# Kernel optimization log

Hardware: AMD Instinct MI355X
Metric: run time of the kernel (lower is better)

## Reference

```python
import jax, jax.numpy as jnp
import numpy as np

S = 4096      # seq_len
D = 1024      # d_model
H = 16        # n_heads
E = 64        # head dim (D // H)
SCALE0 = 1.0 / np.sqrt(E)  # sh_scale_factor


def setup_inputs() -> dict:
    key = jax.random.key(0)
    ks = jax.random.split(key, 10)
    std = 1.0 / np.sqrt(D)
    inputs = jax.random.normal(ks[0], (S, D), dtype=jnp.float32)
    # per-head projection weights stacked over heads: [H, D, E]
    Wq = jax.random.normal(ks[1], (H, D, E), dtype=jnp.float32) * std
    bq = jnp.zeros((H, E), dtype=jnp.float32)
    Wk = jax.random.normal(ks[2], (H, D, E), dtype=jnp.float32) * std
    bk = jnp.zeros((H, E), dtype=jnp.float32)
    Wv = jax.random.normal(ks[3], (H, D, E), dtype=jnp.float32) * std
    bv = jnp.zeros((H, E), dtype=jnp.float32)
    # learned per-head scalar scale, initialized to 1/sqrt(E)
    scale = jnp.full((H,), SCALE0, dtype=jnp.float32)
    # output projection (stored as [D_in, D_out])
    Wo = jax.random.normal(ks[4], (H * E, D), dtype=jnp.float32) * std
    bo = jnp.zeros((D,), dtype=jnp.float32)
    return {"inputs": inputs, "Wq": Wq, "bq": bq, "Wk": Wk, "bk": bk,
            "Wv": Wv, "bv": bv, "scale": scale, "Wo": Wo, "bo": bo}


def reference(inputs, Wq, bq, Wk, bk, Wv, bv, scale, Wo, bo):
    # per-head QKV projections, batched over heads: [H, S, E]
    q = jnp.einsum('sd,hde->hse', inputs, Wq) + bq[:, None, :]
    k = jnp.einsum('sd,hde->hse', inputs, Wk) + bk[:, None, :]
    v = jnp.einsum('sd,hde->hse', inputs, Wv) + bv[:, None, :]
    # scores [H, S, S], learned scalar scale per head, softmax over keys
    scores = jnp.einsum('hqe,hke->hqk', q, k) * scale[:, None, None]
    attn = jax.nn.softmax(scores, axis=-1)
    o = jnp.einsum('hqk,hke->hqe', attn, v)           # [H, S, E]
    o = jnp.transpose(o, (1, 0, 2)).reshape(S, H * E)  # concat heads on dim 1
    return o @ Wo + bo                                 # [S, D]
```

## Files before the change

kernel.cpp:

```cpp
#include <hip/hip_runtime.h>
#include <stdint.h>

#define S_LEN 4096
#define D_MOD 1024
#define NH    16
#define EH    64

typedef short bf16x8 __attribute__((ext_vector_type(8)));
typedef float f32x4  __attribute__((ext_vector_type(4)));
typedef float f32x16 __attribute__((ext_vector_type(16)));

__device__ __forceinline__ unsigned short f2b(float x){
    uint32_t u = __float_as_uint(x);
    u = (u + 0x7fffu + ((u >> 16) & 1u)) >> 16;
    return (unsigned short)u;
}

__device__ __forceinline__ uint32_t cvtpk_bf16(float lo, float hi){
    uint32_t r;
    asm volatile("v_cvt_pk_bf16_f32 %0, %1, %2" : "=v"(r) : "v"(lo), "v"(hi));
    return r;
}

__device__ __forceinline__ void gld_lds16(const void* g, void* l){
    __builtin_amdgcn_global_load_lds((const __attribute__((address_space(1))) void*)g,
                                     (__attribute__((address_space(3))) void*)l, 16, 0, 0);
}

#define PSWAP_U(a, b) asm volatile("v_permlane32_swap_b32 %0, %1" : "+v"(a), "+v"(b))

__device__ __forceinline__ float vcopy(float x){
    float y;
    asm volatile("v_mov_b32 %0, %1" : "=v"(y) : "v"(x));
    return y;
}
__device__ __forceinline__ float pswap_add(float x){
    uint32_t a = __float_as_uint(x), b = __float_as_uint(vcopy(x));
    PSWAP_U(a, b);
    return __uint_as_float(a) + __uint_as_float(b);
}

#define WAITV4() asm volatile("s_waitcnt vmcnt(4)" ::: "memory")
#define WAITV0() asm volatile("s_waitcnt vmcnt(0)" ::: "memory")
#define CFENCE() asm volatile("" ::: "memory")


__global__ void k_conv_all(const float* __restrict__ x, unsigned short* __restrict__ xb,
                           const float* __restrict__ Wq, const float* __restrict__ Wk,
                           const float* __restrict__ Wv, unsigned short* __restrict__ wt,
                           const float* __restrict__ Wo, unsigned short* __restrict__ wot){
    __shared__ float lt[64][65];
    const int tid = threadIdx.x;
    int b = blockIdx.x;
    if (b < 4096){
        int i = (b * 256 + tid) * 4;
        float4 v = *(const float4*)(x + i);
        ushort4 o;
        o.x = f2b(v.x); o.y = f2b(v.y); o.z = f2b(v.z); o.w = f2b(v.w);
        *(ushort4*)(xb + i) = o;
        return;
    }
    b -= 4096;
    if (b < 768){
        const int d0 = (b & 15) * 64;
        const int th = b >> 4;
        const int t = th >> 4, h = th & 15;
        const float* W = (t == 0) ? Wq : ((t == 1) ? Wk : Wv);
        #pragma unroll
        for (int i = 0; i < 16; i++){
            int idx = tid + 256 * i;
            int dl = idx >> 6, e = idx & 63;
            lt[dl][e] = W[((size_t)((h << 10) + d0 + dl) << 6) + e];
        }
        __syncthreads();
        #pragma unroll
        for (int i = 0; i < 16; i++){
            int idx = tid + 256 * i;
            int eo = idx >> 6, dlo = idx & 63;
            wt[((size_t)((t << 10) + (h << 6) + eo) << 10) + d0 + dlo] = f2b(lt[dlo][eo]);
        }
    } else {
        b -= 768;
        const int he0 = (b & 15) * 64, d0 = (b >> 4) * 64;
        #pragma unroll
        for (int i = 0; i < 16; i++){
            int idx = tid + 256 * i;
            int r = idx >> 6, c = idx & 63;
            lt[r][c] = Wo[((size_t)(he0 + r) << 10) + d0 + c];
        }
        __syncthreads();
        #pragma unroll
        for (int i = 0; i < 16; i++){
            int idx = tid + 256 * i;
            int rr = idx >> 6, cc = idx & 63;
            wot[((size_t)(d0 + rr) << 10) + he0 + cc] = f2b(lt[cc][rr]);
        }
    }
}

__global__ void k_tv(const unsigned short* __restrict__ vr, unsigned short* __restrict__ vt){
    __shared__ unsigned short lt[64][66];
    const int tid = threadIdx.x;
    const int s0 = blockIdx.x * 64, h = blockIdx.y;
    #pragma unroll
    for (int i = 0; i < 4; i++){
        int idx = tid + 256 * i;
        int r = idx >> 4, c4 = idx & 15;
        ushort4 v = *(const ushort4*)(vr + (((size_t)(h << 12) + s0 + r) << 6) + c4 * 4);
        lt[r][c4 * 4 + 0] = v.x; lt[r][c4 * 4 + 1] = v.y;
        lt[r][c4 * 4 + 2] = v.z; lt[r][c4 * 4 + 3] = v.w;
    }
    __syncthreads();
    #pragma unroll
    for (int i = 0; i < 4; i++){
        int idx = tid + 256 * i;
        int e = idx >> 4, j4 = idx & 15;
        ushort4 o;
        o.x = lt[j4 * 4 + 0][e]; o.y = lt[j4 * 4 + 1][e];
        o.z = lt[j4 * 4 + 2][e]; o.w = lt[j4 * 4 + 3][e];
        *(ushort4*)(vt + (size_t)((h << 6) + e) * 4096 + s0 + j4 * 4) = o;
    }
}


template<int MODE, int NI>
__global__ __launch_bounds__(256, 4)
void k_gemm(const unsigned short* __restrict__ A, const unsigned short* __restrict__ B, int K,
            unsigned short* __restrict__ qb, unsigned short* __restrict__ kb,
            unsigned short* __restrict__ vr,
            const float* __restrict__ b0, const float* __restrict__ b1, const float* __restrict__ b2,
            const float* __restrict__ scl,
            float* __restrict__ outp, const float* __restrict__ bo){
    __shared__ uint4 lsA4[1024];
    __shared__ uint4 lsB4[NI * 256];
    char* lsA = (char*)lsA4;
    char* lsB = (char*)lsB4;
    const int tid = threadIdx.x;
    const int lane = tid & 63, w = tid >> 6;
    const int lr = lane & 15, lg = lane >> 4;
    const int wm = w >> 1, wn = w & 1;

    const int nwg = gridDim.x * gridDim.y;
    int wgid = blockIdx.y * gridDim.x + blockIdx.x;
    wgid = (wgid & 7) * (nwg >> 3) + (wgid >> 3);
    const int bx = wgid % gridDim.x, by = wgid / gridDim.x;

    const int m0 = by * 128, n0 = bx * (32 * NI);
    const int wbase = tid & ~63;

    f32x4 acc[4][NI] = {};

    for (int k0 = 0; k0 < K; k0 += 64){
        __syncthreads();
        #pragma unroll
        for (int i = 0; i < 4; i++){
            int s = tid + 256 * i;
            int row = s >> 3, c = s & 7;
            int cs = c ^ (row & 7);
            gld_lds16(A + (size_t)(m0 + row) * K + k0 + cs * 8, lsA + (wbase + 256 * i) * 16);
        }
        #pragma unroll
        for (int i = 0; i < NI; i++){
            int s = tid + 256 * i;
            int row = s >> 3, c = s & 7;
            int cs = c ^ (row & 7);
            gld_lds16(B + (size_t)(n0 + row) * K + k0 + cs * 8, lsB + (wbase + 256 * i) * 16);
        }
        __syncthreads();
        #pragma unroll
        for (int kc = 0; kc < 2; kc++){
            bf16x8 af[4], bf[NI];
            #pragma unroll
            for (int mi = 0; mi < 4; mi++){
                int row = wm * 64 + mi * 16 + lr;
                int j = kc * 4 + lg;
                af[mi] = *(const bf16x8*)(lsA + row * 128 + (j ^ (row & 7)) * 16);
            }
            #pragma unroll
            for (int ni = 0; ni < NI; ni++){
                int row = wn * (NI * 16) + ni * 16 + lr;
                int j = kc * 4 + lg;
                bf[ni] = *(const bf16x8*)(lsB + row * 128 + (j ^ (row & 7)) * 16);
            }
            #pragma unroll
            for (int mi = 0; mi < 4; mi++)
                #pragma unroll
                for (int ni = 0; ni < NI; ni++)
                    acc[mi][ni] = __builtin_amdgcn_mfma_f32_16x16x32_bf16(af[mi], bf[ni], acc[mi][ni], 0, 0, 0);
        }
    }

    #pragma unroll
    for (int mi = 0; mi < 4; mi++){
        #pragma unroll
        for (int ni = 0; ni < NI; ni++){
            int gnb = n0 + wn * (NI * 16) + ni * 16;
            if (MODE == 0){
                int t = gnb >> 10, h = (gnb >> 6) & 15;
                int e = (gnb & 63) + lr;
                const float* bp = (t == 0) ? b0 : ((t == 1) ? b1 : b2);
                float badd = bp[(h << 6) + e];
                float qs = (t == 0) ? scl[h] * 1.4426950408889634f : 1.0f;
                unsigned short* tgt = (t == 0) ? qb : ((t == 1) ? kb : vr);
                #pragma unroll
                for (int r = 0; r < 4; r++){
                    int gm = m0 + wm * 64 + mi * 16 + lg * 4 + r;
                    tgt[((size_t)((h << 12) + gm) << 6) + e] = f2b((acc[mi][ni][r] + badd) * qs);
                }
            } else {
                int gn = gnb + lr;
                float badd = bo[gn];
                #pragma unroll
                for (int r = 0; r < 4; r++){
                    int gm = m0 + wm * 64 + mi * 16 + lg * 4 + r;
                    outp[(size_t)gm * 1024 + gn] = acc[mi][ni][r] + badd;
                }
            }
        }
    }
}


__global__ __launch_bounds__(256, 2)
void k_attn(const unsigned short* __restrict__ qb, const unsigned short* __restrict__ kb,
            const unsigned short* __restrict__ vt,
            unsigned short* __restrict__ po0, unsigned short* __restrict__ po1,
            float* __restrict__ pl){
    __shared__ uint4 ldsb[2048];
    char* ldsc = (char*)ldsb;

    const int tid = threadIdx.x;
    const int lane = tid & 63, w = tid >> 6;
    const int ql = lane & 31, hi = lane >> 5;

    int wg = blockIdx.y * 32 + blockIdx.x;
    wg = (wg & 7) * 64 + (wg >> 3);
    const int h = wg >> 5;
    const int rem = wg & 31;
    const int qblk = rem >> 1, sk = rem & 1;
    const int q0 = qblk * 256 + w * 64;
    const int kbase = sk * 2048;

    bf16x8 qf0[4], qf1[4];
    #pragma unroll
    for (int kc = 0; kc < 4; kc++){
        qf0[kc] = *(const bf16x8*)(qb + (size_t)((h << 12) + q0 + ql) * 64 + kc * 16 + hi * 8);
        qf1[kc] = *(const bf16x8*)(qb + (size_t)((h << 12) + q0 + 32 + ql) * 64 + kc * 16 + hi * 8);
    }

    f32x16 o00 = {}, o01 = {}, o10 = {}, o11 = {};
    float ps0 = 0.f, ps1 = 0.f;

    auto stage = [&](int buf, int kt){
        char* Kd = ldsc + buf * 16384;
        char* Vd = Kd + 8192;
        #pragma unroll
        for (int c = 0; c < 2; c++){
            int g = w * 2 + c;
            const unsigned short* ksrc = kb + ((size_t)(h << 12) + kt + (g >> 2) * 32 + ql) * 64
                                            + (g & 3) * 16 + hi * 8;
            gld_lds16(ksrc, Kd + g * 1024);
            const unsigned short* vsrc = vt + (size_t)((h << 6) + (g >> 2) * 32 + ql) * 4096
                                            + kt + (g & 3) * 16 + hi * 8;
            gld_lds16(vsrc, Vd + g * 1024);
        }
    };

    auto pack2 = [&](f32x16& v, bf16x8& pA, bf16x8& pB, float& psum){
        #pragma unroll
        for (int r = 0; r < 16; r++){
            v[r] = __builtin_amdgcn_exp2f(v[r]);
            psum += v[r];
        }
        uint32_t a0 = cvtpk_bf16(v[0], v[1]);
        uint32_t a1 = cvtpk_bf16(v[2], v[3]);
        uint32_t b0 = cvtpk_bf16(v[4], v[5]);
        uint32_t b1 = cvtpk_bf16(v[6], v[7]);
        PSWAP_U(a0, b0);
        PSWAP_U(a1, b1);
        uint32_t f0[4] = {a0, a1, b0, b1};
        pA = *(bf16x8*)f0;
        uint32_t c0 = cvtpk_bf16(v[8],  v[9]);
        uint32_t c1 = cvtpk_bf16(v[10], v[11]);
        uint32_t d0 = cvtpk_bf16(v[12], v[13]);
        uint32_t d1 = cvtpk_bf16(v[14], v[15]);
        PSWAP_U(c0, d0);
        PSWAP_U(c1, d1);
        uint32_t f1[4] = {c0, c1, d0, d1};
        pB = *(bf16x8*)f1;
    };

    stage(0, kbase);
    stage(1, kbase + 64);

    int buf = 0;
    for (int t = 0; t < 32; t++){
        if (t < 31) WAITV4();
        else        WAITV0();
        __builtin_amdgcn_s_barrier();
        CFENCE();

        const char* Kc = ldsc + buf * 16384;
        const char* Vc = Kc + 8192;

        __builtin_amdgcn_s_setprio(1);
        f32x16 s00 = {}, s10 = {};
        #pragma unroll
        for (int kc = 0; kc < 4; kc++){
            bf16x8 kf = *(const bf16x8*)(Kc + kc * 1024 + lane * 16);
            s00 = __builtin_amdgcn_mfma_f32_32x32x16_bf16(kf, qf0[kc], s00, 0, 0, 0);
            s10 = __builtin_amdgcn_mfma_f32_32x32x16_bf16(kf, qf1[kc], s10, 0, 0, 0);
        }
        f32x16 s01 = {}, s11 = {};
        #pragma unroll
        for (int kc = 0; kc < 4; kc++){
            bf16x8 kf = *(const bf16x8*)(Kc + (4 + kc) * 1024 + lane * 16);
            s01 = __builtin_amdgcn_mfma_f32_32x32x16_bf16(kf, qf0[kc], s01, 0, 0, 0);
            s11 = __builtin_amdgcn_mfma_f32_32x32x16_bf16(kf, qf1[kc], s11, 0, 0, 0);
        }
        bf16x8 pA0, pA1, pB0, pB1;
        pack2(s00, pA0, pA1, ps0);
        pack2(s10, pB0, pB1, ps1);

        {
            bf16x8 vf;
            vf = *(const bf16x8*)(Vc + (0 * 4 + 0) * 1024 + lane * 16);
            o00 = __builtin_amdgcn_mfma_f32_32x32x16_bf16(vf, pA0, o00, 0, 0, 0);
            o10 = __builtin_amdgcn_mfma_f32_32x32x16_bf16(vf, pB0, o10, 0, 0, 0);
            vf = *(const bf16x8*)(Vc + (1 * 4 + 0) * 1024 + lane * 16);
            o01 = __builtin_amdgcn_mfma_f32_32x32x16_bf16(vf, pA0, o01, 0, 0, 0);
            o11 = __builtin_amdgcn_mfma_f32_32x32x16_bf16(vf, pB0, o11, 0, 0, 0);
            vf = *(const bf16x8*)(Vc + (0 * 4 + 1) * 1024 + lane * 16);
            o00 = __builtin_amdgcn_mfma_f32_32x32x16_bf16(vf, pA1, o00, 0, 0, 0);
            o10 = __builtin_amdgcn_mfma_f32_32x32x16_bf16(vf, pB1, o10, 0, 0, 0);
            vf = *(const bf16x8*)(Vc + (1 * 4 + 1) * 1024 + lane * 16);
            o01 = __builtin_amdgcn_mfma_f32_32x32x16_bf16(vf, pA1, o01, 0, 0, 0);
            o11 = __builtin_amdgcn_mfma_f32_32x32x16_bf16(vf, pB1, o11, 0, 0, 0);
        }
        bf16x8 pA2, pA3, pB2, pB3;
        pack2(s01, pA2, pA3, ps0);
        pack2(s11, pB2, pB3, ps1);

        {
            bf16x8 vf;
            vf = *(const bf16x8*)(Vc + (0 * 4 + 2) * 1024 + lane * 16);
            o00 = __builtin_amdgcn_mfma_f32_32x32x16_bf16(vf, pA2, o00, 0, 0, 0);
            o10 = __builtin_amdgcn_mfma_f32_32x32x16_bf16(vf, pB2, o10, 0, 0, 0);
            vf = *(const bf16x8*)(Vc + (1 * 4 + 2) * 1024 + lane * 16);
            o01 = __builtin_amdgcn_mfma_f32_32x32x16_bf16(vf, pA2, o01, 0, 0, 0);
            o11 = __builtin_amdgcn_mfma_f32_32x32x16_bf16(vf, pB2, o11, 0, 0, 0);
            vf = *(const bf16x8*)(Vc + (0 * 4 + 3) * 1024 + lane * 16);
            o00 = __builtin_amdgcn_mfma_f32_32x32x16_bf16(vf, pA3, o00, 0, 0, 0);
            o10 = __builtin_amdgcn_mfma_f32_32x32x16_bf16(vf, pB3, o10, 0, 0, 0);
            vf = *(const bf16x8*)(Vc + (1 * 4 + 3) * 1024 + lane * 16);
            o01 = __builtin_amdgcn_mfma_f32_32x32x16_bf16(vf, pA3, o01, 0, 0, 0);
            o11 = __builtin_amdgcn_mfma_f32_32x32x16_bf16(vf, pB3, o11, 0, 0, 0);
        }
        __builtin_amdgcn_s_setprio(0);
        CFENCE();

        if (t + 2 < 32){
            __builtin_amdgcn_s_barrier();
            CFENCE();
            stage(buf, kbase + (t + 2) * 64);
        }
        buf ^= 1;
    }

    unsigned short* pout = sk ? po1 : po0;
    float l0 = pswap_add(ps0);
    float l1 = pswap_add(ps1);
    if (lane < 32){
        pl[((sk << 4) + h) * 4096 + q0 + ql]      = l0;
        pl[((sk << 4) + h) * 4096 + q0 + 32 + ql] = l1;
    }
    #pragma unroll
    for (int hf = 0; hf < 2; hf++){
        int qrow = q0 + hf * 32 + ql;
        #pragma unroll
        for (int et = 0; et < 2; et++){
            const f32x16& o = hf ? (et ? o11 : o10) : (et ? o01 : o00);
            #pragma unroll
            for (int g = 0; g < 4; g++){
                ushort4 o4;
                o4.x = f2b(o[4 * g + 0]);
                o4.y = f2b(o[4 * g + 1]);
                o4.z = f2b(o[4 * g + 2]);
                o4.w = f2b(o[4 * g + 3]);
                int e = et * 32 + 8 * g + 4 * hi;
                *(ushort4*)(pout + (size_t)qrow * 1024 + (h << 6) + e) = o4;
            }
        }
    }
}

__global__ void k_comb(const unsigned short* __restrict__ po0, const unsigned short* __restrict__ po1,
                       const float* __restrict__ pl, unsigned short* __restrict__ ob){
    int i = blockIdx.x * 256 + threadIdx.x;
    int s = i >> 7, g8 = i & 127;
    int h = g8 >> 3;
    float inv = 1.0f / (pl[(h << 12) + s] + pl[((16 + h) << 12) + s]);
    size_t off = ((size_t)s << 10) + g8 * 8;
    const ushort4* a = (const ushort4*)(po0 + off);
    const ushort4* b = (const ushort4*)(po1 + off);
    ushort4 o[2];
    #pragma unroll
    for (int k = 0; k < 2; k++){
        ushort4 av = a[k], bv = b[k];
        o[k].x = f2b((__uint_as_float((uint32_t)av.x << 16) + __uint_as_float((uint32_t)bv.x << 16)) * inv);
        o[k].y = f2b((__uint_as_float((uint32_t)av.y << 16) + __uint_as_float((uint32_t)bv.y << 16)) * inv);
        o[k].z = f2b((__uint_as_float((uint32_t)av.z << 16) + __uint_as_float((uint32_t)bv.z << 16)) * inv);
        o[k].w = f2b((__uint_as_float((uint32_t)av.w << 16) + __uint_as_float((uint32_t)bv.w << 16)) * inv);
    }
    *(ushort4*)(ob + off) = o[0];
    *(ushort4*)(ob + off + 4) = o[1];
}


extern "C" void kernel_launch(void* const* d_in, const int* in_sizes, int n_in,
                              void* d_out, int out_size, void* d_ws, size_t ws_size,
                              hipStream_t stream){
    const float* x  = (const float*)d_in[0];
    const float* Wq = (const float*)d_in[1];
    const float* bq = (const float*)d_in[2];
    const float* Wk = (const float*)d_in[3];
    const float* bk = (const float*)d_in[4];
    const float* Wv = (const float*)d_in[5];
    const float* bv = (const float*)d_in[6];
    const float* sc = (const float*)d_in[7];
    const float* Wo = (const float*)d_in[8];
    const float* bo = (const float*)d_in[9];
    float* out = (float*)d_out;
    char* ws = (char*)d_ws;
    const size_t MB = 1u << 20;

    unsigned short* xb  = (unsigned short*)(ws + 0);
    unsigned short* ob  = xb;
    unsigned short* wt  = (unsigned short*)(ws + 8  * MB);
    unsigned short* wot = (unsigned short*)(ws + 14 * MB);
    unsigned short* qb  = (unsigned short*)(ws + 16 * MB);
    unsigned short* kb  = (unsigned short*)(ws + 24 * MB);
    unsigned short* vr  = (unsigned short*)(ws + 32 * MB);
    unsigned short* po0 = vr;
    unsigned short* vt  = (unsigned short*)(ws + 40 * MB);
    unsigned short* po1 = (unsigned short*)(ws + 48 * MB);
    float*          pl  = (float*)(ws + 56 * MB);

    k_conv_all<<<5120, 256, 0, stream>>>(x, xb, Wq, Wk, Wv, wt, Wo, wot);

    k_gemm<0, 4><<<dim3(24, 32), 256, 0, stream>>>(xb, wt, D_MOD, qb, kb, vr, bq, bk, bv, sc, nullptr, nullptr);
    k_tv        <<<dim3(64, 16), 256, 0, stream>>>(vr, vt);
    k_attn      <<<dim3(32, 16), 256, 0, stream>>>(qb, kb, vt, po0, po1, pl);
    k_comb      <<<2048, 256, 0, stream>>>(po0, po1, pl, ob);
    k_gemm<1, 2><<<dim3(16, 32), 256, 0, stream>>>(ob, wot, D_MOD, nullptr, nullptr, nullptr,
                                                   nullptr, nullptr, nullptr, nullptr, out, bo);
}
```

Before: 142.9 us.

## Fuse V transpose into QKV GEMM epilogue and deepen attention KV tiles

The QKV projection GEMM now writes the V output transposed directly through an LDS staging buffer, so the separate k_tv transpose kernel and its global round trip are removed. The attention kernel stages 128 keys per iteration instead of 64, doubling the LDS buffers. Its QK/PV schedule is also restructured so the next chunk's QK^T overlaps the current chunk's PV. The tradeoffs are higher LDS use, which may lower occupancy, and more live registers in the software-pipelined loop.

After: 149.7 us. 1.05x slower.

```diff
diff --git a/kernel.cpp b/kernel.cpp
--- a/kernel.cpp
+++ b/kernel.cpp
@@ -40,7 +40,7 @@
     return __uint_as_float(a) + __uint_as_float(b);
 }
 
-#define WAITV4() asm volatile("s_waitcnt vmcnt(4)" ::: "memory")
+#define WAITV8() asm volatile("s_waitcnt vmcnt(8)" ::: "memory")
 #define WAITV0() asm volatile("s_waitcnt vmcnt(0)" ::: "memory")
 #define CFENCE() asm volatile("" ::: "memory")
 
@@ -98,43 +98,18 @@
     }
 }
 
-__global__ void k_tv(const unsigned short* __restrict__ vr, unsigned short* __restrict__ vt){
-    __shared__ unsigned short lt[64][66];
-    const int tid = threadIdx.x;
-    const int s0 = blockIdx.x * 64, h = blockIdx.y;
-    #pragma unroll
-    for (int i = 0; i < 4; i++){
-        int idx = tid + 256 * i;
-        int r = idx >> 4, c4 = idx & 15;
-        ushort4 v = *(const ushort4*)(vr + (((size_t)(h << 12) + s0 + r) << 6) + c4 * 4);
-        lt[r][c4 * 4 + 0] = v.x; lt[r][c4 * 4 + 1] = v.y;
-        lt[r][c4 * 4 + 2] = v.z; lt[r][c4 * 4 + 3] = v.w;
-    }
-    __syncthreads();
-    #pragma unroll
-    for (int i = 0; i < 4; i++){
-        int idx = tid + 256 * i;
-        int e = idx >> 4, j4 = idx & 15;
-        ushort4 o;
-        o.x = lt[j4 * 4 + 0][e]; o.y = lt[j4 * 4 + 1][e];
-        o.z = lt[j4 * 4 + 2][e]; o.w = lt[j4 * 4 + 3][e];
-        *(ushort4*)(vt + (size_t)((h << 6) + e) * 4096 + s0 + j4 * 4) = o;
-    }
-}
-
 
 template<int MODE, int NI>
 __global__ __launch_bounds__(256, 4)
 void k_gemm(const unsigned short* __restrict__ A, const unsigned short* __restrict__ B, int K,
             unsigned short* __restrict__ qb, unsigned short* __restrict__ kb,
-            unsigned short* __restrict__ vr,
+            unsigned short* __restrict__ vt,
             const float* __restrict__ b0, const float* __restrict__ b1, const float* __restrict__ b2,
             const float* __restrict__ scl,
             float* __restrict__ outp, const float* __restrict__ bo){
-    __shared__ uint4 lsA4[1024];
-    __shared__ uint4 lsB4[NI * 256];
-    char* lsA = (char*)lsA4;
-    char* lsB = (char*)lsB4;
+    __shared__ uint4 shbuf4[(MODE == 0) ? 2176 : 1536];
+    char* lsA = (char*)shbuf4;
+    char* lsB = (char*)shbuf4 + 16384;
     const int tid = threadIdx.x;
     const int lane = tid & 63, w = tid >> 6;
     const int lr = lane & 15, lg = lane >> 4;
@@ -190,6 +165,39 @@
         }
     }
 
+    if (MODE == 0 && n0 >= 2048){
+        __syncthreads();
+        unsigned short* ldsT = (unsigned short*)shbuf4;
+        #pragma unroll
+        for (int mi = 0; mi < 4; mi++){
+            #pragma unroll
+            for (int ni = 0; ni < NI; ni++){
+                int n_local = wn * (NI * 16) + ni * 16 + lr;
+                int n_global = n0 + n_local;
+                int hh = (n_global >> 6) & 15, e = n_global & 63;
+                float badd = b2[(hh << 6) + e];
+                int m_base = wm * 64 + mi * 16 + lg * 4;
+                ushort4 v4;
+                v4.x = f2b(acc[mi][ni][0] + badd);
+                v4.y = f2b(acc[mi][ni][1] + badd);
+                v4.z = f2b(acc[mi][ni][2] + badd);
+                v4.w = f2b(acc[mi][ni][3] + badd);
+                *(ushort4*)(ldsT + n_local * 136 + m_base) = v4;
+            }
+        }
+        __syncthreads();
+        #pragma unroll
+        for (int i = 0; i < 8; i++){
+            int idx = tid + 256 * i;
+            int r = idx >> 4, chunk = idx & 15;
+            int n_global = n0 + r;
+            int hh = (n_global >> 6) & 15, e = n_global & 63;
+            uint4 vv = *(const uint4*)(ldsT + r * 136 + chunk * 8);
+            *(uint4*)(vt + (size_t)((hh << 6) + e) * 4096 + m0 + chunk * 8) = vv;
+        }
+        return;
+    }
+
     #pragma unroll
     for (int mi = 0; mi < 4; mi++){
         #pragma unroll
@@ -198,10 +206,10 @@
             if (MODE == 0){
                 int t = gnb >> 10, h = (gnb >> 6) & 15;
                 int e = (gnb & 63) + lr;
-                const float* bp = (t == 0) ? b0 : ((t == 1) ? b1 : b2);
+                const float* bp = (t == 0) ? b0 : b1;
                 float badd = bp[(h << 6) + e];
                 float qs = (t == 0) ? scl[h] * 1.4426950408889634f : 1.0f;
-                unsigned short* tgt = (t == 0) ? qb : ((t == 1) ? kb : vr);
+                unsigned short* tgt = (t == 0) ? qb : kb;
                 #pragma unroll
                 for (int r = 0; r < 4; r++){
                     int gm = m0 + wm * 64 + mi * 16 + lg * 4 + r;
@@ -226,7 +234,7 @@
             const unsigned short* __restrict__ vt,
             unsigned short* __restrict__ po0, unsigned short* __restrict__ po1,
             float* __restrict__ pl){
-    __shared__ uint4 ldsb[2048];
+    __shared__ uint4 ldsb[4096];
     char* ldsc = (char*)ldsb;
 
     const int tid = threadIdx.x;
@@ -252,16 +260,16 @@
     float ps0 = 0.f, ps1 = 0.f;
 
     auto stage = [&](int buf, int kt){
-        char* Kd = ldsc + buf * 16384;
-        char* Vd = Kd + 8192;
-        #pragma unroll
-        for (int c = 0; c < 2; c++){
-            int g = w * 2 + c;
+        char* Kd = ldsc + buf * 32768;
+        char* Vd = Kd + 16384;
+        #pragma unroll
+        for (int c = 0; c < 4; c++){
+            int g = w * 4 + c;
             const unsigned short* ksrc = kb + ((size_t)(h << 12) + kt + (g >> 2) * 32 + ql) * 64
                                             + (g & 3) * 16 + hi * 8;
             gld_lds16(ksrc, Kd + g * 1024);
-            const unsigned short* vsrc = vt + (size_t)((h << 6) + (g >> 2) * 32 + ql) * 4096
-                                            + kt + (g & 3) * 16 + hi * 8;
+            const unsigned short* vsrc = vt + (size_t)((h << 6) + (g >> 3) * 32 + ql) * 4096
+                                            + kt + (g & 7) * 16 + hi * 8;
             gld_lds16(vsrc, Vd + g * 1024);
         }
     };
@@ -291,78 +299,76 @@
     };
 
     stage(0, kbase);
-    stage(1, kbase + 64);
+    stage(1, kbase + 128);
 
     int buf = 0;
-    for (int t = 0; t < 32; t++){
-        if (t < 31) WAITV4();
+    for (int t = 0; t < 16; t++){
+        if (t < 15) WAITV8();
         else        WAITV0();
         __builtin_amdgcn_s_barrier();
         CFENCE();
 
-        const char* Kc = ldsc + buf * 16384;
-        const char* Vc = Kc + 8192;
-
-        __builtin_amdgcn_s_setprio(1);
-        f32x16 s00 = {}, s10 = {};
-        #pragma unroll
-        for (int kc = 0; kc < 4; kc++){
-            bf16x8 kf = *(const bf16x8*)(Kc + kc * 1024 + lane * 16);
-            s00 = __builtin_amdgcn_mfma_f32_32x32x16_bf16(kf, qf0[kc], s00, 0, 0, 0);
-            s10 = __builtin_amdgcn_mfma_f32_32x32x16_bf16(kf, qf1[kc], s10, 0, 0, 0);
-        }
-        f32x16 s01 = {}, s11 = {};
-        #pragma unroll
-        for (int kc = 0; kc < 4; kc++){
-            bf16x8 kf = *(const bf16x8*)(Kc + (4 + kc) * 1024 + lane * 16);
-            s01 = __builtin_amdgcn_mfma_f32_32x32x16_bf16(kf, qf0[kc], s01, 0, 0, 0);
-            s11 = __builtin_amdgcn_mfma_f32_32x32x16_bf16(kf, qf1[kc], s11, 0, 0, 0);
-        }
-        bf16x8 pA0, pA1, pB0, pB1;
-        pack2(s00, pA0, pA1, ps0);
-        pack2(s10, pB0, pB1, ps1);
-
-        {
+        const char* Kc = ldsc + buf * 32768;
+        const char* Vc = Kc + 16384;
+
+        auto qkt = [&](int qq, f32x16& sv0, f32x16& sv1){
+            #pragma unroll
+            for (int kc = 0; kc < 4; kc++){
+                bf16x8 kf = *(const bf16x8*)(Kc + (qq * 4 + kc) * 1024 + lane * 16);
+                sv0 = __builtin_amdgcn_mfma_f32_32x32x16_bf16(kf, qf0[kc], sv0, 0, 0, 0);
+                sv1 = __builtin_amdgcn_mfma_f32_32x32x16_bf16(kf, qf1[kc], sv1, 0, 0, 0);
+            }
+        };
+        auto pv = [&](int qq, bf16x8 pA0, bf16x8 pA1, bf16x8 pB0, bf16x8 pB1){
             bf16x8 vf;
-            vf = *(const bf16x8*)(Vc + (0 * 4 + 0) * 1024 + lane * 16);
+            vf = *(const bf16x8*)(Vc + (0 * 8 + 2 * qq) * 1024 + lane * 16);
             o00 = __builtin_amdgcn_mfma_f32_32x32x16_bf16(vf, pA0, o00, 0, 0, 0);
             o10 = __builtin_amdgcn_mfma_f32_32x32x16_bf16(vf, pB0, o10, 0, 0, 0);
-            vf = *(const bf16x8*)(Vc + (1 * 4 + 0) * 1024 + lane * 16);
+            vf = *(const bf16x8*)(Vc + (1 * 8 + 2 * qq) * 1024 + lane * 16);
             o01 = __builtin_amdgcn_mfma_f32_32x32x16_bf16(vf, pA0, o01, 0, 0, 0);
             o11 = __builtin_amdgcn_mfma_f32_32x32x16_bf16(vf, pB0, o11, 0, 0, 0);
-            vf = *(const bf16x8*)(Vc + (0 * 4 + 1) * 1024 + lane * 16);
+            vf = *(const bf16x8*)(Vc + (0 * 8 + 2 * qq + 1) * 1024 + lane * 16);
             o00 = __builtin_amdgcn_mfma_f32_32x32x16_bf16(vf, pA1, o00, 0, 0, 0);
             o10 = __builtin_amdgcn_mfma_f32_32x32x16_bf16(vf, pB1, o10, 0, 0, 0);
-            vf = *(const bf16x8*)(Vc + (1 * 4 + 1) * 1024 + lane * 16);
+            vf = *(const bf16x8*)(Vc + (1 * 8 + 2 * qq + 1) * 1024 + lane * 16);
             o01 = __builtin_amdgcn_mfma_f32_32x32x16_bf16(vf, pA1, o01, 0, 0, 0);
             o11 = __builtin_amdgcn_mfma_f32_32x32x16_bf16(vf, pB1, o11, 0, 0, 0);
-        }
-        bf16x8 pA2, pA3, pB2, pB3;
-        pack2(s01, pA2, pA3, ps0);
-        pack2(s11, pB2, pB3, ps1);
-
+        };
+
+        __builtin_amdgcn_s_setprio(1);
+        bf16x8 pA0, pA1, pB0, pB1;
         {
-            bf16x8 vf;
-            vf = *(const bf16x8*)(Vc + (0 * 4 + 2) * 1024 + lane * 16);
-            o00 = __builtin_amdgcn_mfma_f32_32x32x16_bf16(vf, pA2, o00, 0, 0, 0);
-            o10 = __builtin_amdgcn_mfma_f32_32x32x16_bf16(vf, pB2, o10, 0, 0, 0);
-            vf = *(const bf16x8*)(Vc + (1 * 4 + 2) * 1024 + lane * 16);
-            o01 = __builtin_amdgcn_mfma_f32_32x32x16_bf16(vf, pA2, o01, 0, 0, 0);
-            o11 = __builtin_amdgcn_mfma_f32_32x32x16_bf16(vf, pB2, o11, 0, 0, 0);
-            vf = *(const bf16x8*)(Vc + (0 * 4 + 3) * 1024 + lane * 16);
-            o00 = __builtin_amdgcn_mfma_f32_32x32x16_bf16(vf, pA3, o00, 0, 0, 0);
-            o10 = __builtin_amdgcn_mfma_f32_32x32x16_bf16(vf, pB3, o10, 0, 0, 0);
-            vf = *(const bf16x8*)(Vc + (1 * 4 + 3) * 1024 + lane * 16);
-            o01 = __builtin_amdgcn_mfma_f32_32x32x16_bf16(vf, pA3, o01, 0, 0, 0);
-            o11 = __builtin_amdgcn_mfma_f32_32x32x16_bf16(vf, pB3, o11, 0, 0, 0);
+            f32x16 s00 = {}, s10 = {}, s01 = {}, s11 = {};
+            qkt(0, s00, s10);
+            qkt(1, s01, s11);
+            pack2(s00, pA0, pA1, ps0);
+            pack2(s10, pB0, pB1, ps1);
+            pv(0, pA0, pA1, pB0, pB1);
+            pack2(s01, pA0, pA1, ps0);
+            pack2(s11, pB0, pB1, ps1);
+        }
+        {
+            f32x16 s02 = {}, s12 = {};
+            qkt(2, s02, s12);
+            pv(1, pA0, pA1, pB0, pB1);
+            pack2(s02, pA0, pA1, ps0);
+            pack2(s12, pB0, pB1, ps1);
+        }
+        {
+            f32x16 s03 = {}, s13 = {};
+            qkt(3, s03, s13);
+            pv(2, pA0, pA1, pB0, pB1);
+            pack2(s03, pA0, pA1, ps0);
+            pack2(s13, pB0, pB1, ps1);
+            pv(3, pA0, pA1, pB0, pB1);
         }
         __builtin_amdgcn_s_setprio(0);
         CFENCE();
 
-        if (t + 2 < 32){
+        if (t + 2 < 16){
             __builtin_amdgcn_s_barrier();
             CFENCE();
-            stage(buf, kbase + (t + 2) * 64);
+            stage(buf, kbase + (t + 2) * 128);
         }
         buf ^= 1;
     }
@@ -440,16 +446,14 @@
     unsigned short* wot = (unsigned short*)(ws + 14 * MB);
     unsigned short* qb  = (unsigned short*)(ws + 16 * MB);
     unsigned short* kb  = (unsigned short*)(ws + 24 * MB);
-    unsigned short* vr  = (unsigned short*)(ws + 32 * MB);
-    unsigned short* po0 = vr;
+    unsigned short* po0 = (unsigned short*)(ws + 32 * MB);
     unsigned short* vt  = (unsigned short*)(ws + 40 * MB);
     unsigned short* po1 = (unsigned short*)(ws + 48 * MB);
     float*          pl  = (float*)(ws + 56 * MB);
 
     k_conv_all<<<5120, 256, 0, stream>>>(x, xb, Wq, Wk, Wv, wt, Wo, wot);
 
-    k_gemm<0, 4><<<dim3(24, 32), 256, 0, stream>>>(xb, wt, D_MOD, qb, kb, vr, bq, bk, bv, sc, nullptr, nullptr);
-    k_tv        <<<dim3(64, 16), 256, 0, stream>>>(vr, vt);
+    k_gemm<0, 4><<<dim3(24, 32), 256, 0, stream>>>(xb, wt, D_MOD, qb, kb, vt, bq, bk, bv, sc, nullptr, nullptr);
     k_attn      <<<dim3(32, 16), 256, 0, stream>>>(qb, kb, vt, po0, po1, pl);
     k_comb      <<<2048, 256, 0, stream>>>(po0, po1, pl, ob);
     k_gemm<1, 2><<<dim3(16, 32), 256, 0, stream>>>(ob, wot, D_MOD, nullptr, nullptr, nullptr,
```
